# Performance work log

Measured on AMD Instinct MI355X. Metric: run time of the kernel, lower is better.

The kernel has to match this reference:

```python
import jax, jax.numpy as jnp
import numpy as np

DIM, HEADS, DHEAD = 256, 8, 64
HID = HEADS * DHEAD


def _elu1(x):
    # F.elu(x) + 1 == exp(x) for x<0, x+1 for x>=0
    return jnp.where(x > 0, x + 1.0, jnp.exp(x))


def setup_inputs() -> dict:
    key = jax.random.key(0)
    ks = jax.random.split(key, 6)
    B, H, W = 8, 64, 64
    x = jax.random.normal(ks[0], (B, DIM, H, W), dtype=jnp.float32)
    contact_map = jax.random.uniform(ks[1], (B, 1, H, W), dtype=jnp.float32)
    s_qkv = 1.0 / np.sqrt(DIM)
    Wqkv = jax.random.normal(ks[2], (3 * HID, DIM), dtype=jnp.float32) * s_qkv
    s_out = 1.0 / np.sqrt(HID)
    Wout = jax.random.normal(ks[3], (DIM, HID), dtype=jnp.float32) * s_out
    bout = jax.random.normal(ks[4], (DIM,), dtype=jnp.float32) * 0.01
    contact_scale = jnp.float32(0.1)
    return {"x": x, "contact_map": contact_map, "Wqkv": Wqkv,
            "Wout": Wout, "bout": bout, "contact_scale": contact_scale}


def reference(x, contact_map, Wqkv, Wout, bout, contact_scale):
    b, c, h, w = x.shape
    n = h * w
    xf = x.reshape(b, c, n)                                  # b c n
    qkv = jnp.einsum('oc,bcn->bon', Wqkv, xf)                # b (3*H*D) n
    qkv = qkv.reshape(b, 3, HEADS, DHEAD, n)                 # qkv-major channel order
    q = _elu1(qkv[:, 0])                                     # b h d n
    k = _elu1(qkv[:, 1])
    v = qkv[:, 2]
    cm = contact_map.reshape(b, 1, 1, n)                     # b 1 1 n
    k = k * (1.0 + contact_scale * cm)
    kv = jnp.einsum('bhdn,bhen->bhde', k, v)                 # b h d e
    ksum = k.sum(axis=-1)                                    # b h d
    z = 1.0 / (jnp.einsum('bhdn,bhd->bhn', q, ksum) + 1e-6)  # b h n
    out = jnp.einsum('bhde,bhdn->bhne', kv, q) * z[..., None]  # b h n e
    out = out.transpose(0, 1, 3, 2).reshape(b, HID, n)       # b (h d) n
    y = jnp.einsum('oc,bcn->bon', Wout, out) + bout[None, :, None]
    return y.reshape(b, -1, h, w)
```

## Files before the change

kernel.cpp:

```cpp
#include <hip/hip_runtime.h>
#include <stdint.h>


#define NPIX 4096
#define HIDC 512
#define DIMC 256
#define BATCH 8

typedef __attribute__((ext_vector_type(8))) short bf16x8;
typedef __attribute__((ext_vector_type(4))) float f32x4;
typedef __attribute__((ext_vector_type(16))) float f32x16;

__device__ __forceinline__ float bf2f(unsigned short h) {
    unsigned int u = ((unsigned int)h) << 16; float f;
    __builtin_memcpy(&f, &u, 4); return f;
}
__device__ __forceinline__ unsigned short f2bf(float f) {
    unsigned int u; __builtin_memcpy(&u, &f, 4);
    u += 0x7fffu + ((u >> 16) & 1u);
    return (unsigned short)(u >> 16);
}
__device__ __forceinline__ float elu1(float x) {
    return x > 0.f ? x + 1.f : __expf(x);
}
__device__ __forceinline__ void gl16(const unsigned short* g, unsigned short* l) {
    __builtin_amdgcn_global_load_lds(
        (__attribute__((address_space(1))) const void*)g,
        (__attribute__((address_space(3))) void*)l, 16, 0, 0);
}

__global__ __launch_bounds__(256) void k_convW(
    const float* __restrict__ Wqkv, const float* __restrict__ Wout,
    unsigned short* __restrict__ Wb, unsigned short* __restrict__ Wpo)
{
    int i4 = (blockIdx.x * 256 + threadIdx.x) * 4;
    const int NW1 = 1536 * 256;
    if (i4 < NW1) {
        float4 v = *(const float4*)&Wqkv[i4];
        ushort4 u; u.x = f2bf(v.x); u.y = f2bf(v.y); u.z = f2bf(v.z); u.w = f2bf(v.w);
        *(ushort4*)&Wb[i4] = u;
    } else {
        int jj = i4 - NW1;
        float4 v = *(const float4*)&Wout[jj];
        ushort4 u; u.x = f2bf(v.x); u.y = f2bf(v.y); u.z = f2bf(v.z); u.w = f2bf(v.w);
        const int o = jj >> 9, c = jj & 511;
        const int og = o >> 5, l31 = o & 31;
        const int ks = c >> 4, lhi = (c >> 3) & 1, j = c & 7;
        *(ushort4*)&Wpo[og * 16384 + ks * 512 + (l31 * 2 + lhi) * 8 + j] = u;
    }
}

__global__ __launch_bounds__(256) void k_tx(
    const float* __restrict__ x, unsigned short* __restrict__ xT)
{
    __shared__ float tile[32][33];
    const int n0 = blockIdx.x * 32, c0 = blockIdx.y * 32, b = blockIdx.z;
    const int t = threadIdx.x;
    const int r = t >> 3, c4 = (t & 7) * 4;
    float4 v = *(const float4*)&x[((size_t)b * DIMC + c0 + r) * NPIX + n0 + c4];
    tile[r][c4 + 0] = v.x; tile[r][c4 + 1] = v.y;
    tile[r][c4 + 2] = v.z; tile[r][c4 + 3] = v.w;
    __syncthreads();
    ushort4 o;
    unsigned short* op = (unsigned short*)&o;
#pragma unroll
    for (int i = 0; i < 4; i++) op[i] = f2bf(tile[c4 + i][r]);
    *(ushort4*)&xT[((size_t)b * NPIX + n0 + r) * DIMC + c0 + c4] = o;
}

__global__ __launch_bounds__(256) void k_fused(
    const unsigned short* __restrict__ xT,
    const unsigned short* __restrict__ Wb,
    const float* __restrict__ cmp,
    const float* __restrict__ csp,
    unsigned short* __restrict__ qT,
    float* __restrict__ kvq,
    float* __restrict__ ksump)
{
    const int b  = blockIdx.z;
    const int m0 = blockIdx.x * 128;
    const int yb = blockIdx.y;
    const int h  = yb - 4;
    const int t = threadIdx.x;
    const int wave = t >> 6, lane = t & 63;
    const int wm = wave >> 1, wn = wave & 1;
    const int l31 = lane & 31, lhi = lane >> 5;

    __shared__ unsigned short sh[128 * 128];
    unsigned short* As  = sh;
    unsigned short* Bs  = sh + 128 * 64;
    unsigned short* kvS = sh;

    const unsigned short* Ag = xT + ((size_t)b * NPIX + m0) * DIMC;

    f32x16 acc[2][2];
#pragma unroll
    for (int i = 0; i < 2; i++)
#pragma unroll
        for (int j = 0; j < 2; j++)
#pragma unroll
            for (int r = 0; r < 16; r++) acc[i][j][r] = 0.f;

    const int r8  = lane >> 3;
    const int jg8 = (((lane & 7) ^ r8) & 7) * 8;
    const int xsw = (l31 & 7);

    for (int k0 = 0; k0 < DIMC; k0 += 64) {
#pragma unroll
        for (int i = 0; i < 4; i++) {
            const int rowg = wave * 32 + i * 8;
            const int arow = rowg + r8;
            gl16(&Ag[(size_t)arow * DIMC + k0 + jg8], &As[rowg * 64]);
            int wrow;
            if (yb < 4) wrow = yb * 128 + arow;
            else wrow = (arow < 64) ? (512 + h * 64 + arow)
                                    : (1024 + h * 64 + (arow - 64));
            gl16(&Wb[(size_t)wrow * DIMC + k0 + jg8], &Bs[rowg * 64]);
        }
        __syncthreads();
#pragma unroll
        for (int ks = 0; ks < 4; ks++) {
            const int coff = ((ks * 2 + lhi) ^ xsw) * 8;
            bf16x8 af[2], bfg[2];
#pragma unroll
            for (int fm = 0; fm < 2; fm++)
                af[fm] = *(const bf16x8*)&As[(wm * 64 + fm * 32 + l31) * 64 + coff];
#pragma unroll
            for (int fn = 0; fn < 2; fn++)
                bfg[fn] = *(const bf16x8*)&Bs[(wn * 64 + fn * 32 + l31) * 64 + coff];
#pragma unroll
            for (int fm = 0; fm < 2; fm++)
#pragma unroll
                for (int fn = 0; fn < 2; fn++)
                    acc[fm][fn] = __builtin_amdgcn_mfma_f32_32x32x16_bf16(
                        af[fm], bfg[fn], acc[fm][fn], 0, 0, 0);
        }
        __syncthreads();
    }

    if (yb < 4) {
        const int n0 = yb * 128;
#pragma unroll
        for (int fm = 0; fm < 2; fm++) {
            const int pbase = m0 + wm * 64 + fm * 32;
#pragma unroll
            for (int fn = 0; fn < 2; fn++) {
                const int o = n0 + wn * 64 + fn * 32 + l31;
#pragma unroll
                for (int r = 0; r < 16; r++) {
                    int prow = pbase + (r & 3) + 8 * (r >> 2) + 4 * lhi;
                    qT[((size_t)b * NPIX + prow) * HIDC + o] = f2bf(elu1(acc[fm][fn][r]));
                }
            }
        }
        return;
    }

    const float cs = *csp;
    const bool isK = (wn == 0);
    float gv4[2];
#pragma unroll
    for (int fm = 0; fm < 2; fm++)
        gv4[fm] = 1.f + cs * cmp[(size_t)b * NPIX + m0 + wm * 64 + fm * 32 + l31];

    float gk[2][16];
#pragma unroll
    for (int fm = 0; fm < 2; fm++)
#pragma unroll
        for (int r = 0; r < 16; r++)
            gk[fm][r] = __shfl(gv4[fm], (r & 3) + 8 * (r >> 2) + 4 * lhi);

    float ks0 = 0.f, ks1 = 0.f;
#pragma unroll
    for (int fm = 0; fm < 2; fm++) {
#pragma unroll
        for (int fn = 0; fn < 2; fn++) {
            const int o = wn * 64 + fn * 32 + l31;
            const int sw = (o & 7) << 3;
#pragma unroll
            for (int rg = 0; rg < 4; rg++) {
                ushort4 pk4;
                unsigned short* pp = (unsigned short*)&pk4;
#pragma unroll
                for (int j = 0; j < 4; j++) {
                    const int r = rg * 4 + j;
                    float val = acc[fm][fn][r];
                    if (isK) {
                        float kvl = elu1(val) * gk[fm][r];
                        if (fn == 0) ks0 += kvl; else ks1 += kvl;
                        pp[j] = f2bf(kvl);
                    } else {
                        pp[j] = f2bf(val);
                    }
                }
                const int px0 = wm * 64 + fm * 32 + rg * 8 + 4 * lhi;
                *(ushort4*)&kvS[(size_t)o * 128 + (px0 ^ sw)] = pk4;
            }
        }
    }
    if (isK) {
        atomicAdd(&ksump[(size_t)(b * 8 + h) * 64 + l31], ks0);
        atomicAdd(&ksump[(size_t)(b * 8 + h) * 64 + 32 + l31], ks1);
    }
    __syncthreads();

    f32x16 kva;
#pragma unroll
    for (int r = 0; r < 16; r++) kva[r] = 0.f;
#pragma unroll
    for (int pk = 0; pk < 8; pk++) {
        const int co = ((pk * 2 + lhi) ^ (l31 & 7)) * 8;
        bf16x8 kf = *(const bf16x8*)&kvS[(size_t)(wm * 32 + l31) * 128 + co];
        bf16x8 vf = *(const bf16x8*)&kvS[(size_t)(64 + wn * 32 + l31) * 128 + co];
        kva = __builtin_amdgcn_mfma_f32_32x32x16_bf16(kf, vf, kva, 0, 0, 0);
    }
    float* kvb = kvq + ((size_t)(b * 8 + h) * 32 + blockIdx.x) * 4096;
#pragma unroll
    for (int r = 0; r < 16; r++) {
        const int d = wm * 32 + (r & 3) + 8 * (r >> 2) + 4 * lhi;
        kvb[(size_t)d * 64 + wn * 32 + l31] = kva[r];
    }
}

__global__ __launch_bounds__(256) void k_kvred(
    const float* __restrict__ kvq, float* __restrict__ kvp)
{
    const int bh = blockIdx.x >> 2, q4 = blockIdx.x & 3;
    const float4* src = (const float4*)(kvq + (size_t)bh * 32 * 4096)
                      + q4 * 256 + threadIdx.x;
    float4 s; s.x = 0.f; s.y = 0.f; s.z = 0.f; s.w = 0.f;
#pragma unroll 8
    for (int i = 0; i < 32; i++) {
        float4 v = src[(size_t)i * 1024];
        s.x += v.x; s.y += v.y; s.z += v.z; s.w += v.w;
    }
    ((float4*)(kvp + (size_t)bh * 4096))[q4 * 256 + threadIdx.x] = s;
}

__global__ __launch_bounds__(256, 2) void k_oy(
    const unsigned short* __restrict__ qT,
    const float* __restrict__ kvp,
    const float* __restrict__ ksum,
    const unsigned short* __restrict__ Wpo,
    const float* __restrict__ bout,
    float* __restrict__ y)
{
    const int b  = blockIdx.y;
    const int px0 = blockIdx.x * 64;
    const int t = threadIdx.x;
    const int wave = t >> 6, lane = t & 63;
    const int pxh = wave & 1, whi = wave >> 1;
    const int l31 = lane & 31, lhi = lane >> 5;
    const int lidx = (l31 * 2 + lhi) * 8;

    __shared__ unsigned short qS[2][64 * 64];
    __shared__ unsigned short kvS2[64 * 72];
    __shared__ unsigned short outS[64 * 64];
    __shared__ float ksS[64];

    const int r8 = lane >> 3;
    const int jg8 = ((lane & 7) ^ r8) * 8;

    auto stageQ = [&](int h, int buf) {
        const unsigned short* qg = qT + ((size_t)b * NPIX + px0) * HIDC + h * 64;
#pragma unroll
        for (int i = 0; i < 2; i++) {
            const int rowb = wave * 16 + i * 8;
            gl16(&qg[(size_t)(rowb + r8) * HIDC + jg8], &qS[buf][rowb * 64]);
        }
    };
    auto stageKV = [&](int h) {
        const float* kvg = kvp + (size_t)(b * 8 + h) * 4096;
#pragma unroll
        for (int i = 0; i < 16; i++) {
            int idx = t + i * 256;
            int d = idx >> 6, e = idx & 63;
            kvS2[e * 72 + d] = f2bf(kvg[idx]);
        }
        if (t < 64) ksS[t] = ksum[(size_t)(b * 8 + h) * 64 + t];
    };

    stageQ(0, 0);
    stageKV(0);

    f32x16 yacc[4];
#pragma unroll
    for (int mt = 0; mt < 4; mt++)
#pragma unroll
        for (int r = 0; r < 16; r++) yacc[mt][r] = 0.f;

    int cur = 0;
    __syncthreads();

#pragma unroll 1
    for (int h = 0; h < 8; h++) {
        bf16x8 qf[4];
#pragma unroll
        for (int s = 0; s < 4; s++)
            qf[s] = *(const bf16x8*)&qS[cur][(pxh * 32 + l31) * 64
                                            + (((s * 2 + lhi) ^ (l31 & 7)) * 8)];
        f32x16 oacc;
#pragma unroll
        for (int r = 0; r < 16; r++) oacc[r] = 0.f;
#pragma unroll
        for (int s = 0; s < 4; s++) {
            bf16x8 kvf = *(const bf16x8*)&kvS2[(whi * 32 + l31) * 72 + s * 16 + lhi * 8];
            oacc = __builtin_amdgcn_mfma_f32_32x32x16_bf16(kvf, qf[s], oacc, 0, 0, 0);
        }
        float den = 0.f;
#pragma unroll
        for (int s = 0; s < 4; s++) {
            f32x4 ka = *(const f32x4*)&ksS[s * 16 + lhi * 8];
            f32x4 kb = *(const f32x4*)&ksS[s * 16 + lhi * 8 + 4];
            const unsigned short* qp = (const unsigned short*)&qf[s];
#pragma unroll
            for (int j = 0; j < 4; j++) {
                den += bf2f(qp[j]) * ka[j];
                den += bf2f(qp[4 + j]) * kb[j];
            }
        }
        den += __shfl_xor(den, 32);
        const float z = 1.f / (den + 1e-6f);

        ushort4 op4[4];
#pragma unroll
        for (int rg = 0; rg < 4; rg++) {
            unsigned short* pp = (unsigned short*)&op4[rg];
#pragma unroll
            for (int j = 0; j < 4; j++)
                pp[j] = f2bf(oacc[rg * 4 + j] * z);
        }

        __syncthreads();
        {
            const int px = pxh * 32 + l31;
#pragma unroll
            for (int rg = 0; rg < 4; rg++)
                *(ushort4*)&outS[px * 64 + (((whi * 4 + rg) ^ (px & 7)) * 8) + 4 * lhi]
                    = op4[rg];
        }
        if (h < 7) { stageQ(h + 1, cur ^ 1); stageKV(h + 1); }
        __syncthreads();

#pragma unroll
        for (int k16 = 0; k16 < 4; k16++) {
            const int px = pxh * 32 + l31;
            bf16x8 of = *(const bf16x8*)&outS[px * 64 + (((k16 * 2 + lhi) ^ (px & 7)) * 8)];
#pragma unroll
            for (int mt = 0; mt < 4; mt++) {
                bf16x8 wf = *(const bf16x8*)&Wpo[(size_t)(whi * 4 + mt) * 16384
                                                 + (h * 4 + k16) * 512 + lidx];
                yacc[mt] = __builtin_amdgcn_mfma_f32_32x32x16_bf16(wf, of, yacc[mt], 0, 0, 0);
            }
        }
        cur ^= 1;
    }

#pragma unroll
    for (int mt = 0; mt < 4; mt++) {
#pragma unroll
        for (int r = 0; r < 16; r++) {
            const int o = whi * 128 + mt * 32 + (r & 3) + 8 * (r >> 2) + 4 * lhi;
            y[((size_t)b * DIMC + o) * NPIX + px0 + pxh * 32 + l31]
                = yacc[mt][r] + bout[o];
        }
    }
}

extern "C" void kernel_launch(void* const* d_in, const int* in_sizes, int n_in,
                              void* d_out, int out_size, void* d_ws, size_t ws_size,
                              hipStream_t stream) {
    (void)in_sizes; (void)n_in; (void)out_size; (void)ws_size;
    const float* x    = (const float*)d_in[0];
    const float* cm   = (const float*)d_in[1];
    const float* Wqkv = (const float*)d_in[2];
    const float* Wout = (const float*)d_in[3];
    const float* bout = (const float*)d_in[4];
    const float* csp  = (const float*)d_in[5];
    float* y = (float*)d_out;

    const size_t qn = (size_t)BATCH * HIDC * NPIX;
    char* ws = (char*)d_ws;
    unsigned short* qT   = (unsigned short*)ws;                 ws += qn * 2;
    unsigned short* xT   = (unsigned short*)ws;                 ws += qn * 2;
    float* kvp   = (float*)ws;                                  ws += (size_t)64 * 64 * 64 * 4;
    float* ksump = (float*)ws;                                  ws += (size_t)64 * 64 * 4;
    float* kvq   = (float*)ws;                                  ws += (size_t)64 * 32 * 4096 * 4;
    unsigned short* Wb  = (unsigned short*)ws;                  ws += (size_t)1536 * 256 * 2;
    unsigned short* Wpo = (unsigned short*)ws;

    hipMemsetAsync(ksump, 0, (size_t)64 * 64 * sizeof(float), stream);
    k_convW<<<512, 256, 0, stream>>>(Wqkv, Wout, Wb, Wpo);
    k_tx   <<<dim3(128, 8, 8), 256, 0, stream>>>(x, xT);
    k_fused<<<dim3(32, 12, 8), 256, 0, stream>>>(xT, Wb, cm, csp, qT, kvq, ksump);
    k_kvred<<<256, 256, 0, stream>>>(kvq, kvp);
    k_oy   <<<dim3(64, 8),     256, 0, stream>>>(qT, kvp, ksump, Wpo, bout, y);
}
```

Baseline: 199.9 us.

## Fuse Q, K and V projection per head into one 128x192 GEMM tile

Each block now computes the Q, K and V projections for one head over 128 pixels (N=192), where before Q and KV were handled by separate blocks. The x tile is loaded once per head instead of being reloaded by separate Q blocks, the grid shrinks from 12 to 8 y-blocks, and the load imbalance between Q-only and KV blocks goes away. In exchange each thread holds 6 accumulator tiles, which raises register pressure and may lower occupancy, and LDS use grows to 40KB.

```diff
diff --git a/kernel.cpp b/kernel.cpp
--- a/kernel.cpp
+++ b/kernel.cpp
@@ -78,26 +78,25 @@
     float* __restrict__ ksump)
 {
     const int b  = blockIdx.z;
+    const int h  = blockIdx.y;
     const int m0 = blockIdx.x * 128;
-    const int yb = blockIdx.y;
-    const int h  = yb - 4;
     const int t = threadIdx.x;
     const int wave = t >> 6, lane = t & 63;
     const int wm = wave >> 1, wn = wave & 1;
     const int l31 = lane & 31, lhi = lane >> 5;
 
-    __shared__ unsigned short sh[128 * 128];
+    __shared__ unsigned short sh[320 * 64];
     unsigned short* As  = sh;
     unsigned short* Bs  = sh + 128 * 64;
     unsigned short* kvS = sh;
 
     const unsigned short* Ag = xT + ((size_t)b * NPIX + m0) * DIMC;
 
-    f32x16 acc[2][2];
+    f32x16 acc[2][3];
 #pragma unroll
     for (int i = 0; i < 2; i++)
 #pragma unroll
-        for (int j = 0; j < 2; j++)
+        for (int j = 0; j < 3; j++)
 #pragma unroll
             for (int r = 0; r < 16; r++) acc[i][j][r] = 0.f;
 
@@ -109,99 +108,95 @@
 #pragma unroll
         for (int i = 0; i < 4; i++) {
             const int rowg = wave * 32 + i * 8;
-            const int arow = rowg + r8;
-            gl16(&Ag[(size_t)arow * DIMC + k0 + jg8], &As[rowg * 64]);
-            int wrow;
-            if (yb < 4) wrow = yb * 128 + arow;
-            else wrow = (arow < 64) ? (512 + h * 64 + arow)
-                                    : (1024 + h * 64 + (arow - 64));
-            gl16(&Wb[(size_t)wrow * DIMC + k0 + jg8], &Bs[rowg * 64]);
+            gl16(&Ag[(size_t)(rowg + r8) * DIMC + k0 + jg8], &As[rowg * 64]);
+        }
+#pragma unroll
+        for (int i = 0; i < 6; i++) {
+            const int rowb = wave * 48 + i * 8;
+            const int arow = rowb + r8;
+            const int wrow = (arow < 64)  ? (h * 64 + arow)
+                           : (arow < 128) ? (512 + h * 64 + (arow - 64))
+                                          : (1024 + h * 64 + (arow - 128));
+            gl16(&Wb[(size_t)wrow * DIMC + k0 + jg8], &Bs[rowb * 64]);
         }
         __syncthreads();
 #pragma unroll
         for (int ks = 0; ks < 4; ks++) {
             const int coff = ((ks * 2 + lhi) ^ xsw) * 8;
-            bf16x8 af[2], bfg[2];
+            bf16x8 af[2], bfg[3];
 #pragma unroll
             for (int fm = 0; fm < 2; fm++)
                 af[fm] = *(const bf16x8*)&As[(wm * 64 + fm * 32 + l31) * 64 + coff];
 #pragma unroll
-            for (int fn = 0; fn < 2; fn++)
-                bfg[fn] = *(const bf16x8*)&Bs[(wn * 64 + fn * 32 + l31) * 64 + coff];
+            for (int fn = 0; fn < 3; fn++)
+                bfg[fn] = *(const bf16x8*)&Bs[(wn * 96 + fn * 32 + l31) * 64 + coff];
 #pragma unroll
             for (int fm = 0; fm < 2; fm++)
 #pragma unroll
-                for (int fn = 0; fn < 2; fn++)
+                for (int fn = 0; fn < 3; fn++)
                     acc[fm][fn] = __builtin_amdgcn_mfma_f32_32x32x16_bf16(
                         af[fm], bfg[fn], acc[fm][fn], 0, 0, 0);
         }
         __syncthreads();
     }
 
-    if (yb < 4) {
-        const int n0 = yb * 128;
-#pragma unroll
-        for (int fm = 0; fm < 2; fm++) {
-            const int pbase = m0 + wm * 64 + fm * 32;
-#pragma unroll
-            for (int fn = 0; fn < 2; fn++) {
-                const int o = n0 + wn * 64 + fn * 32 + l31;
+    const float cs = *csp;
+    float gv4[2];
+#pragma unroll
+    for (int fm = 0; fm < 2; fm++)
+        gv4[fm] = 1.f + cs * cmp[(size_t)b * NPIX + m0 + wm * 64 + fm * 32 + l31];
+
+    float gk[2][16];
+#pragma unroll
+    for (int fm = 0; fm < 2; fm++)
+#pragma unroll
+        for (int r = 0; r < 16; r++)
+            gk[fm][r] = __shfl(gv4[fm], (r & 3) + 8 * (r >> 2) + 4 * lhi);
+
+    float ksl = 0.f;
+#pragma unroll
+    for (int fn = 0; fn < 3; fn++) {
+        const int ct = wn * 3 + fn;
+        if (ct <= 1) {
+            const int o = h * 64 + ct * 32 + l31;
+#pragma unroll
+            for (int fm = 0; fm < 2; fm++) {
+                const int pbase = m0 + wm * 64 + fm * 32;
 #pragma unroll
                 for (int r = 0; r < 16; r++) {
                     int prow = pbase + (r & 3) + 8 * (r >> 2) + 4 * lhi;
                     qT[((size_t)b * NPIX + prow) * HIDC + o] = f2bf(elu1(acc[fm][fn][r]));
                 }
             }
-        }
-        return;
-    }
-
-    const float cs = *csp;
-    const bool isK = (wn == 0);
-    float gv4[2];
-#pragma unroll
-    for (int fm = 0; fm < 2; fm++)
-        gv4[fm] = 1.f + cs * cmp[(size_t)b * NPIX + m0 + wm * 64 + fm * 32 + l31];
-
-    float gk[2][16];
-#pragma unroll
-    for (int fm = 0; fm < 2; fm++)
-#pragma unroll
-        for (int r = 0; r < 16; r++)
-            gk[fm][r] = __shfl(gv4[fm], (r & 3) + 8 * (r >> 2) + 4 * lhi);
-
-    float ks0 = 0.f, ks1 = 0.f;
-#pragma unroll
-    for (int fm = 0; fm < 2; fm++) {
-#pragma unroll
-        for (int fn = 0; fn < 2; fn++) {
-            const int o = wn * 64 + fn * 32 + l31;
+        } else {
+            const int o = (ct - 2) * 32 + l31;
+            const bool isK = (ct <= 3);
             const int sw = (o & 7) << 3;
 #pragma unroll
-            for (int rg = 0; rg < 4; rg++) {
-                ushort4 pk4;
-                unsigned short* pp = (unsigned short*)&pk4;
-#pragma unroll
-                for (int j = 0; j < 4; j++) {
-                    const int r = rg * 4 + j;
-                    float val = acc[fm][fn][r];
-                    if (isK) {
-                        float kvl = elu1(val) * gk[fm][r];
-                        if (fn == 0) ks0 += kvl; else ks1 += kvl;
-                        pp[j] = f2bf(kvl);
-                    } else {
-                        pp[j] = f2bf(val);
+            for (int fm = 0; fm < 2; fm++) {
+#pragma unroll
+                for (int rg = 0; rg < 4; rg++) {
+                    ushort4 pk4;
+                    unsigned short* pp = (unsigned short*)&pk4;
+#pragma unroll
+                    for (int j = 0; j < 4; j++) {
+                        const int r = rg * 4 + j;
+                        float val = acc[fm][fn][r];
+                        if (isK) {
+                            float kvl = elu1(val) * gk[fm][r];
+                            ksl += kvl;
+                            pp[j] = f2bf(kvl);
+                        } else {
+                            pp[j] = f2bf(val);
+                        }
                     }
+                    const int px0 = wm * 64 + fm * 32 + rg * 8 + 4 * lhi;
+                    *(ushort4*)&kvS[(size_t)o * 128 + (px0 ^ sw)] = pk4;
                 }
-                const int px0 = wm * 64 + fm * 32 + rg * 8 + 4 * lhi;
-                *(ushort4*)&kvS[(size_t)o * 128 + (px0 ^ sw)] = pk4;
             }
         }
     }
-    if (isK) {
-        atomicAdd(&ksump[(size_t)(b * 8 + h) * 64 + l31], ks0);
-        atomicAdd(&ksump[(size_t)(b * 8 + h) * 64 + 32 + l31], ks1);
-    }
+    atomicAdd(&ksump[(size_t)(b * 8 + h) * 64 + wn * 32 + l31], ksl);
     __syncthreads();
 
     f32x16 kva;
@@ -392,7 +387,7 @@
     hipMemsetAsync(ksump, 0, (size_t)64 * 64 * sizeof(float), stream);
     k_convW<<<512, 256, 0, stream>>>(Wqkv, Wout, Wb, Wpo);
     k_tx   <<<dim3(128, 8, 8), 256, 0, stream>>>(x, xT);
-    k_fused<<<dim3(32, 12, 8), 256, 0, stream>>>(xT, Wb, cm, csp, qT, kvq, ksump);
+    k_fused<<<dim3(32, 8, 8),  256, 0, stream>>>(xT, Wb, cm, csp, qT, kvq, ksump);
     k_kvred<<<256, 256, 0, stream>>>(kvq, kvp);
     k_oy   <<<dim3(64, 8),     256, 0, stream>>>(qT, kvp, ksump, Wpo, bout, y);
 }
```

After: 222.3 us. 11.2% more time.
